# Kernel optimization log

Measured on AMD Instinct MI355X. Metric: run time of the kernel, lower is better.

## Reference

```python
import jax, jax.numpy as jnp
import numpy as np

B, H, W, C = 32, 32, 32, 512
N_GROUPS = 32
EPS = 1e-5


def group_norm(x, scale, bias, n_groups=N_GROUPS, eps=EPS):
    b, h, w, c = x.shape
    xg = x.reshape(b, h, w, n_groups, c // n_groups)
    mean = xg.mean(axis=(1, 2, 4), keepdims=True)
    var = xg.var(axis=(1, 2, 4), keepdims=True)
    xg = (xg - mean) * jax.lax.rsqrt(var + eps)
    return xg.reshape(b, h, w, c) * scale + bias


def setup_inputs() -> dict:
    key = jax.random.key(0)
    ks = jax.random.split(key, 8)
    x = jax.random.normal(ks[0], (B, H, W, C), dtype=jnp.float32)
    t = jax.random.normal(ks[1], (B,), dtype=jnp.float32)
    gn_scale = jnp.ones((C,), jnp.float32)
    gn_bias = jnp.zeros((C,), jnp.float32)
    w_qkv = jax.random.normal(ks[2], (C, 3 * C), dtype=jnp.float32) / np.sqrt(C)
    b_qkv = jnp.zeros((3 * C,), jnp.float32)
    w_out = jax.random.normal(ks[3], (C, C), dtype=jnp.float32) / np.sqrt(C)
    b_out = jnp.zeros((C,), jnp.float32)
    return {"x": x, "t": t, "gn_scale": gn_scale, "gn_bias": gn_bias,
            "w_qkv": w_qkv, "b_qkv": b_qkv, "w_out": w_out, "b_out": b_out}


def reference(x, t, gn_scale, gn_bias, w_qkv, b_qkv, w_out, b_out):
    b, h, w, c = x.shape
    z = group_norm(x, gn_scale, gn_bias)
    qkv = jnp.einsum('bhwc,cd->bhwd', z, w_qkv) + b_qkv  # [b,h,w,3C]
    q, k, v = jnp.split(qkv, 3, axis=-1)
    # single-head spatial attention over all h*w positions
    attn = jnp.einsum('bhwc,bHWc->bhwHW', q, k) / jnp.sqrt(jnp.asarray(c, x.dtype))
    attn = jax.nn.softmax(attn.reshape(b, h, w, h * w), axis=-1)
    attn = attn.reshape(b, h, w, h, w)
    scores = jnp.einsum('bhwHW,bHWc->bhwc', attn, v)
    scores = jnp.einsum('bhwc,cd->bhwd', scores, w_out) + b_out
    return x + scores
```

## Files before the change

### kernel.cpp

```cpp
#include <hip/hip_runtime.h>

typedef unsigned short u16;
typedef short bf16x8 __attribute__((ext_vector_type(8)));
typedef float f32x4 __attribute__((ext_vector_type(4)));

__device__ __forceinline__ u16 f2bf(float f) {
  union { float f; unsigned u; } c; c.f = f;
  unsigned r = (c.u + 0x7FFFu + ((c.u >> 16) & 1u)) >> 16;
  return (u16)r;
}
__device__ __forceinline__ float bf2f(u16 h) {
  union { unsigned u; float f; } c; c.u = ((unsigned)h) << 16;
  return c.f;
}
__device__ __forceinline__ void gload16(const void* g, void* l) {
  __builtin_amdgcn_global_load_lds(
      (const __attribute__((address_space(1))) unsigned*)g,
      (__attribute__((address_space(3))) unsigned*)l, 16, 0, 0);
}

__global__ __launch_bounds__(256) void prep_weights(
    const float* __restrict__ w_qkv, const float* __restrict__ w_out,
    u16* __restrict__ wqkvT, u16* __restrict__ woutT) {
  int i = blockIdx.x * 256 + threadIdx.x;
  const int T1 = 1536 * 512;
  if (i < T1) {
    int n = i >> 9, c = i & 511;
    wqkvT[i] = f2bf(w_qkv[(size_t)c * 1536 + n]);
  } else {
    int j = i - T1;
    int n = j >> 9, c = j & 511;
    woutT[j] = f2bf(w_out[(size_t)c * 512 + n]);
  }
}

__global__ __launch_bounds__(256) void groupnorm_k(
    const float* __restrict__ x, const float* __restrict__ scale,
    const float* __restrict__ bias, u16* __restrict__ z) {
  const int blk = blockIdx.x, b = blk >> 5, g = blk & 31;
  const float* xb = x + (size_t)b * 524288 + g * 16;
  u16* zb = z + (size_t)b * 524288 + g * 16;
  const int tid = threadIdx.x, lane = tid & 63, wid = tid >> 6;

  float4 vv[16];
  float s = 0.f, ss = 0.f;
#pragma unroll
  for (int i = 0; i < 16; ++i) {
    int e = (i * 256 + tid) * 4;
    int hw = e >> 4, j = e & 15;
    vv[i] = *(const float4*)&xb[(size_t)hw * 512 + j];
    s += vv[i].x + vv[i].y + vv[i].z + vv[i].w;
    ss += vv[i].x * vv[i].x + vv[i].y * vv[i].y + vv[i].z * vv[i].z + vv[i].w * vv[i].w;
  }
#pragma unroll
  for (int off = 32; off; off >>= 1) {
    s += __shfl_xor(s, off);
    ss += __shfl_xor(ss, off);
  }
  __shared__ float rs[4], rq[4];
  if (!lane) { rs[wid] = s; rq[wid] = ss; }
  __syncthreads();
  float S_ = rs[0] + rs[1] + rs[2] + rs[3];
  float Q_ = rq[0] + rq[1] + rq[2] + rq[3];
  const float inv_n = 1.f / 16384.f;
  float mean = S_ * inv_n;
  float var = Q_ * inv_n - mean * mean;
  float rstd = rsqrtf(var + 1e-5f);

  int j0 = (tid * 4) & 15;
  float sc0 = scale[g * 16 + j0 + 0] * rstd, sc1 = scale[g * 16 + j0 + 1] * rstd;
  float sc2 = scale[g * 16 + j0 + 2] * rstd, sc3 = scale[g * 16 + j0 + 3] * rstd;
  float bi0 = bias[g * 16 + j0 + 0] - mean * sc0, bi1 = bias[g * 16 + j0 + 1] - mean * sc1;
  float bi2 = bias[g * 16 + j0 + 2] - mean * sc2, bi3 = bias[g * 16 + j0 + 3] - mean * sc3;
#pragma unroll
  for (int i = 0; i < 16; ++i) {
    int e = (i * 256 + tid) * 4;
    int hw = e >> 4, j = e & 15;
    ushort4 o;
    o.x = f2bf(vv[i].x * sc0 + bi0);
    o.y = f2bf(vv[i].y * sc1 + bi1);
    o.z = f2bf(vv[i].z * sc2 + bi2);
    o.w = f2bf(vv[i].w * sc3 + bi3);
    *(ushort4*)&zb[(size_t)hw * 512 + j] = o;
  }
}

#define QSCALE 0.04419417382415922f

template <int EPI>
__global__ __launch_bounds__(512, 2) void gemm_ring(
    const u16* __restrict__ A, const u16* __restrict__ Bt,
    int gx, int gxy, int N, int K,
    int sched, int sp1, int sp2,
    long long sAb, long long sBb, long long sCb,
    const float* __restrict__ bias, const float* __restrict__ resid,
    u16* __restrict__ qb, u16* __restrict__ kb, u16* __restrict__ vt,
    u16* __restrict__ outb, float* __restrict__ outf) {
  const int orig = blockIdx.x;
  const int xcd = orig & 7, jj = orig >> 3;
  int id;
  if (sched == 0) {
    int pan = jj % gx, loc = jj / gx;
    id = (xcd * sp1 + loc) * gx + pan;
  } else {
    int tile = jj % gxy, bl = jj / gxy;
    id = (xcd * sp2 + bl) * gxy + tile;
  }
  const int z = id / gxy;
  const int r2 = id - z * gxy;
  const int by = r2 / gx, bx = r2 - by * gx;

  const u16* Ab = A + (size_t)z * sAb;
  const u16* Bb = Bt + (size_t)z * sBb;

  __shared__ u16 As[4][8192];
  __shared__ u16 Bs[4][8192];

  const int tid = threadIdx.x;
  const int lane = tid & 63, wid = tid >> 6;
  const int wm = wid & 1, wn = wid >> 1;
  const int l15 = lane & 15, l4 = lane >> 4;
  const int m0 = by * 256, n0 = bx * 256;

  const int lrs = tid >> 3;
  const int g0 = (tid & 7) ^ (lrs & 7);
  const int ra = (lrs << 1) | (g0 >> 2);
  const int ko = (g0 & 3) << 3;

  const int lrb = l15 >> 1;
  const int gg = ((l15 & 1) << 2) | l4;
  const int gsw = gg ^ lrb;
  const int aoff = wm * 4096 + lrb * 64 + gsw * 8;
  const int boff = (wn >> 1) * 4096 + (wn & 1) * 2048 + lrb * 64 + gsw * 8;

  f32x4 acc[8][4];
#pragma unroll
  for (int i = 0; i < 8; ++i)
#pragma unroll
    for (int j = 0; j < 4; ++j)
#pragma unroll
      for (int r = 0; r < 4; ++r) acc[i][j][r] = 0.f;

  const int NT = K >> 5;

  auto stA = [&](int sb, int t2) {
    const u16* s0 = Ab + (size_t)(m0 + ra) * K + t2 * 32 + ko;
    const u16* s1 = Ab + (size_t)(m0 + 128 + ra) * K + t2 * 32 + ko;
    gload16(s0, &As[sb][tid * 8]);
    gload16(s1, &As[sb][4096 + tid * 8]);
  };
  auto stB = [&](int sb, int t2) {
    const u16* s0 = Bb + (size_t)(n0 + ra) * K + t2 * 32 + ko;
    const u16* s1 = Bb + (size_t)(n0 + 128 + ra) * K + t2 * 32 + ko;
    gload16(s0, &Bs[sb][tid * 8]);
    gload16(s1, &Bs[sb][4096 + tid * 8]);
  };

#define TILE_BODY(P, TT, DOSTG, WN)                                            \
  do {                                                                         \
    if (DOSTG) { stA(((P) + 3) & 3, (TT) + 3); stB(((P) + 3) & 3, (TT) + 3); } \
    bf16x8 bq[4], af0[4], af1[4];                                              \
    _Pragma("unroll") for (int ni = 0; ni < 4; ++ni)                           \
        bq[ni] = *(const bf16x8*)&Bs[P][boff + ni * 512];                      \
    _Pragma("unroll") for (int i = 0; i < 4; ++i)                              \
        af0[i] = *(const bf16x8*)&As[P][aoff + i * 512];                       \
    _Pragma("unroll") for (int i = 0; i < 4; ++i)                              \
        af1[i] = *(const bf16x8*)&As[P][aoff + 2048 + i * 512];                \
    __builtin_amdgcn_s_setprio(1);                                             \
    _Pragma("unroll") for (int i = 0; i < 4; ++i)                              \
        _Pragma("unroll") for (int ni = 0; ni < 4; ++ni)                       \
            acc[i][ni] = __builtin_amdgcn_mfma_f32_16x16x32_bf16(              \
                af0[i], bq[ni], acc[i][ni], 0, 0, 0);                          \
    _Pragma("unroll") for (int i = 0; i < 4; ++i)                              \
        _Pragma("unroll") for (int ni = 0; ni < 4; ++ni)                       \
            acc[4 + i][ni] = __builtin_amdgcn_mfma_f32_16x16x32_bf16(          \
                af1[i], bq[ni], acc[4 + i][ni], 0, 0, 0);                      \
    __builtin_amdgcn_s_setprio(0);                                             \
    if ((WN) == 8) asm volatile("s_waitcnt vmcnt(8)" ::: "memory");            \
    else if ((WN) == 4) asm volatile("s_waitcnt vmcnt(4)" ::: "memory");       \
    else if ((WN) == 0) asm volatile("s_waitcnt vmcnt(0)" ::: "memory");       \
    if ((WN) >= -1) __builtin_amdgcn_s_barrier();                              \
  } while (0)

  stA(0, 0); stB(0, 0);
  stA(1, 1); stB(1, 1);
  stA(2, 2); stB(2, 2);
  asm volatile("s_waitcnt vmcnt(8)" ::: "memory");
  __builtin_amdgcn_s_barrier();

  int t = 0;
  for (; t + 7 < NT; t += 4) {
    TILE_BODY(0, t, 1, 8);
    TILE_BODY(1, t + 1, 1, 8);
    TILE_BODY(2, t + 2, 1, 8);
    TILE_BODY(3, t + 3, 1, 8);
  }
  TILE_BODY(0, t, 1, 8);
  TILE_BODY(1, t + 1, 0, 4);
  TILE_BODY(2, t + 2, 0, 0);
  TILE_BODY(3, t + 3, 0, -2);

#undef TILE_BODY

  if (EPI == 0) {
#pragma unroll
    for (int mi = 0; mi < 8; ++mi) {
#pragma unroll
      for (int ni = 0; ni < 4; ++ni) {
        const int gr0 = m0 + wm * 128 + mi * 16 + l4 * 4;
        const int gc = n0 + wn * 64 + ni * 16 + l15;
        const int bsel = gc >> 9, cin = gc & 511;
        const float bs = bias[gc];
        if (bsel < 2) {
          u16* dst = bsel ? kb : qb;
#pragma unroll
          for (int r = 0; r < 4; ++r) {
            float vvv = acc[mi][ni][r] + bs;
            if (bsel == 0) vvv *= QSCALE;
            dst[(size_t)(gr0 + r) * 512 + cin] = f2bf(vvv);
          }
        } else {
          ushort4 o;
          o.x = f2bf(acc[mi][ni][0] + bs);
          o.y = f2bf(acc[mi][ni][1] + bs);
          o.z = f2bf(acc[mi][ni][2] + bs);
          o.w = f2bf(acc[mi][ni][3] + bs);
          const int bb = gr0 >> 10, p = gr0 & 1023;
          *(ushort4*)&vt[(size_t)bb * 524288 + (size_t)cin * 1024 + p] = o;
        }
      }
    }
  } else {
#pragma unroll
    for (int mi = 0; mi < 8; ++mi) {
#pragma unroll
      for (int ni = 0; ni < 4; ++ni) {
        const int gr0 = m0 + wm * 128 + mi * 16 + l4 * 4;
        const int gc = n0 + wn * 64 + ni * 16 + l15;
#pragma unroll
        for (int r = 0; r < 4; ++r)
          outf[(size_t)(gr0 + r) * N + gc] =
              acc[mi][ni][r] + bias[gc] + resid[(size_t)(gr0 + r) * N + gc];
      }
    }
  }
}

__global__ __launch_bounds__(512, 2) void flash_k(
    const u16* __restrict__ qg, const u16* __restrict__ kg,
    const u16* __restrict__ vtg, u16* __restrict__ Og) {
  __shared__ u16 Ks[2][32 * 512];
  __shared__ u16 Ps[2][128 * 40];
  __shared__ float rsumS[128];

  const int tid = threadIdx.x, lane = tid & 63, wid = tid >> 6;
  const int l15 = lane & 15, l4 = lane >> 4;
  const int orig = blockIdx.x;
  const int xcd = orig & 7, jj = orig >> 3;
  const int z = xcd * 4 + (jj & 3);
  const int qb0 = jj >> 2;

  const u16* qz = qg + (size_t)(z * 1024 + qb0 * 128) * 512;
  const u16* kz = kg + (size_t)z * 1024 * 512;
  const u16* vz = vtg + (size_t)z * 512 * 1024;

  const int krow_ = tid >> 6;
  const int kgr = tid & 63;
  const int kgs = (kgr & 56) | ((kgr & 7) ^ (krow_ & 7));

  auto stageK = [&](int t, int buf) {
    const u16* src = kz + ((size_t)t * 32 + krow_) * 512 + kgs * 8;
#pragma unroll
    for (int s = 0; s < 4; ++s)
      gload16(src + (size_t)s * 8 * 512, &Ks[buf][s * 4096 + tid * 8]);
  };

  const int dbase = wid * 64;
  bf16x8 vcur[4], vnxt[4];
  auto loadV = [&](int t, bf16x8* dst) {
#pragma unroll
    for (int nf = 0; nf < 4; ++nf)
      dst[nf] = *(const bf16x8*)&vz[(size_t)(dbase + nf * 16 + l15) * 1024 + t * 32 + l4 * 8];
  };

  bf16x8 qf[16];
#pragma unroll
  for (int kf = 0; kf < 16; ++kf)
    qf[kf] = *(const bf16x8*)&qz[(size_t)(wid * 16 + l15) * 512 + kf * 32 + l4 * 8];

  f32x4 oacc[8][4];
#pragma unroll
  for (int i = 0; i < 8; ++i)
#pragma unroll
    for (int j = 0; j < 4; ++j)
#pragma unroll
      for (int r = 0; r < 4; ++r) oacc[i][j][r] = 0.f;
  float rsum[4] = {0.f, 0.f, 0.f, 0.f};

  stageK(0, 0);
  loadV(0, vcur);
  asm volatile("s_waitcnt vmcnt(4)" ::: "memory");
  __builtin_amdgcn_s_barrier();

  for (int t = 0; t < 32; ++t) {
    const int cur = t & 1;
    const bool pre = (t + 1 < 32);
    if (pre) { stageK(t + 1, cur ^ 1); loadV(t + 1, vnxt); }

    f32x4 sacc[2];
#pragma unroll
    for (int nf = 0; nf < 2; ++nf)
#pragma unroll
      for (int r = 0; r < 4; ++r) sacc[nf][r] = 0.f;
#pragma unroll
    for (int kf = 0; kf < 16; ++kf) {
#pragma unroll
      for (int nf = 0; nf < 2; ++nf) {
        const int kvr = nf * 16 + l15;
        const int g = kf * 4 + l4;
        const int gs = (g & 56) | ((g & 7) ^ (kvr & 7));
        const bf16x8 bfr = *(const bf16x8*)&Ks[cur][kvr * 512 + gs * 8];
        sacc[nf] = __builtin_amdgcn_mfma_f32_16x16x32_bf16(qf[kf], bfr, sacc[nf], 0, 0, 0);
      }
    }

#pragma unroll
    for (int nf = 0; nf < 2; ++nf)
#pragma unroll
      for (int r = 0; r < 4; ++r) {
        const float e = __expf(sacc[nf][r]);
        rsum[r] += e;
        Ps[cur][(wid * 16 + l4 * 4 + r) * 40 + nf * 16 + l15] = f2bf(e);
      }

    if (pre) asm volatile("s_waitcnt vmcnt(4)" ::: "memory");
    __builtin_amdgcn_s_barrier();

    __builtin_amdgcn_s_setprio(1);
#pragma unroll
    for (int mi = 0; mi < 8; ++mi) {
      const bf16x8 pa = *(const bf16x8*)&Ps[cur][(mi * 16 + l15) * 40 + l4 * 8];
#pragma unroll
      for (int nf = 0; nf < 4; ++nf)
        oacc[mi][nf] = __builtin_amdgcn_mfma_f32_16x16x32_bf16(pa, vcur[nf], oacc[mi][nf], 0, 0, 0);
    }
    __builtin_amdgcn_s_setprio(0);

    if (pre) {
#pragma unroll
      for (int nf = 0; nf < 4; ++nf) vcur[nf] = vnxt[nf];
    }
  }

#pragma unroll
  for (int r = 0; r < 4; ++r) {
    float v = rsum[r];
    v += __shfl_xor(v, 1);
    v += __shfl_xor(v, 2);
    v += __shfl_xor(v, 4);
    v += __shfl_xor(v, 8);
    if (l15 == 0) rsumS[wid * 16 + l4 * 4 + r] = 1.0f / v;
  }
  __syncthreads();

  u16* ob = Og + (size_t)(z * 1024 + qb0 * 128) * 512;
#pragma unroll
  for (int mi = 0; mi < 8; ++mi) {
#pragma unroll
    for (int r = 0; r < 4; ++r) {
      const int q = mi * 16 + l4 * 4 + r;
      const float inv = rsumS[q];
#pragma unroll
      for (int nf = 0; nf < 4; ++nf)
        ob[(size_t)q * 512 + dbase + nf * 16 + l15] = f2bf(oacc[mi][nf][r] * inv);
    }
  }
}

extern "C" void kernel_launch(void* const* d_in, const int* in_sizes, int n_in,
                              void* d_out, int out_size, void* d_ws, size_t ws_size,
                              hipStream_t stream) {
  const float* x = (const float*)d_in[0];
  const float* gn_scale = (const float*)d_in[2];
  const float* gn_bias = (const float*)d_in[3];
  const float* w_qkv = (const float*)d_in[4];
  const float* b_qkv = (const float*)d_in[5];
  const float* w_out = (const float*)d_in[6];
  const float* b_out = (const float*)d_in[7];
  float* out = (float*)d_out;

  char* ws = (char*)d_ws;
  const size_t MB = 1024ull * 1024ull;
  u16* qb = (u16*)(ws + 0 * MB);
  u16* kb = (u16*)(ws + 32 * MB);
  u16* vt = (u16*)(ws + 64 * MB);
  u16* zO = (u16*)(ws + 128 * MB);
  u16* wqkvT = (u16*)(ws + 224 * MB);
  u16* woutT = (u16*)(ws + 226 * MB);

  prep_weights<<<4096, 256, 0, stream>>>(w_qkv, w_out, wqkvT, woutT);
  groupnorm_k<<<1024, 256, 0, stream>>>(x, gn_scale, gn_bias, zO);

  gemm_ring<0><<<768, 512, 0, stream>>>(
      zO, wqkvT, 6, 768, 1536, 512, 0, 16, 0, 0, 0, 0, b_qkv, nullptr,
      qb, kb, vt, nullptr, nullptr);

  flash_k<<<256, 512, 0, stream>>>(qb, kb, vt, zO);

  gemm_ring<2><<<256, 512, 0, stream>>>(
      zO, woutT, 2, 256, 512, 512, 0, 16, 0, 0, 0, 0, b_out, x,
      nullptr, nullptr, nullptr, nullptr, out);
}
```

Baseline: 235.0 us.

## Software-pipeline attention loop so QK of tile t overlaps PV of tile t-1

Restructures the attention main loop so that each iteration computes the QK scores for the current K tile and the P·V product for the previous tile's probabilities. This lets the exp/softmax writes and the P·V MFMAs of neighbouring tiles interleave without waiting on each other. The V register double buffer now ping-pongs between two named arrays through a two-way unrolled macro body, which removes the per-iteration register copy. A peeled prologue and epilogue handle the first QK-only step and the final P·V. The extra unrolling may raise register pressure and lengthen the code.

```diff
diff --git a/kernel.cpp b/kernel.cpp
--- a/kernel.cpp
+++ b/kernel.cpp
@@ -276,8 +276,8 @@
   };
 
   const int dbase = wid * 64;
-  bf16x8 vcur[4], vnxt[4];
-  auto loadV = [&](int t, bf16x8* dst) {
+  bf16x8 va[4], vb[4];
+  auto loadV = [&](int t, bf16x8 (&dst)[4]) {
 #pragma unroll
     for (int nf = 0; nf < 4; ++nf)
       dst[nf] = *(const bf16x8*)&vz[(size_t)(dbase + nf * 16 + l15) * 1024 + t * 32 + l4 * 8];
@@ -298,59 +298,65 @@
   float rsum[4] = {0.f, 0.f, 0.f, 0.f};
 
   stageK(0, 0);
-  loadV(0, vcur);
+  loadV(0, vb);
   asm volatile("s_waitcnt vmcnt(4)" ::: "memory");
   __builtin_amdgcn_s_barrier();
 
-  for (int t = 0; t < 32; ++t) {
-    const int cur = t & 1;
-    const bool pre = (t + 1 < 32);
-    if (pre) { stageK(t + 1, cur ^ 1); loadV(t + 1, vnxt); }
-
-    f32x4 sacc[2];
-#pragma unroll
-    for (int nf = 0; nf < 2; ++nf)
-#pragma unroll
-      for (int r = 0; r < 4; ++r) sacc[nf][r] = 0.f;
-#pragma unroll
-    for (int kf = 0; kf < 16; ++kf) {
-#pragma unroll
-      for (int nf = 0; nf < 2; ++nf) {
-        const int kvr = nf * 16 + l15;
-        const int g = kf * 4 + l4;
-        const int gs = (g & 56) | ((g & 7) ^ (kvr & 7));
-        const bf16x8 bfr = *(const bf16x8*)&Ks[cur][kvr * 512 + gs * 8];
-        sacc[nf] = __builtin_amdgcn_mfma_f32_16x16x32_bf16(qf[kf], bfr, sacc[nf], 0, 0, 0);
-      }
-    }
-
-#pragma unroll
-    for (int nf = 0; nf < 2; ++nf)
-#pragma unroll
-      for (int r = 0; r < 4; ++r) {
-        const float e = __expf(sacc[nf][r]);
-        rsum[r] += e;
-        Ps[cur][(wid * 16 + l4 * 4 + r) * 40 + nf * 16 + l15] = f2bf(e);
-      }
-
-    if (pre) asm volatile("s_waitcnt vmcnt(4)" ::: "memory");
-    __builtin_amdgcn_s_barrier();
-
-    __builtin_amdgcn_s_setprio(1);
-#pragma unroll
-    for (int mi = 0; mi < 8; ++mi) {
-      const bf16x8 pa = *(const bf16x8*)&Ps[cur][(mi * 16 + l15) * 40 + l4 * 8];
-#pragma unroll
-      for (int nf = 0; nf < 4; ++nf)
-        oacc[mi][nf] = __builtin_amdgcn_mfma_f32_16x16x32_bf16(pa, vcur[nf], oacc[mi][nf], 0, 0, 0);
-    }
-    __builtin_amdgcn_s_setprio(0);
-
-    if (pre) {
-#pragma unroll
-      for (int nf = 0; nf < 4; ++nf) vcur[nf] = vnxt[nf];
-    }
-  }
+#define FBODY(I, VPV, DOPV, PRE)                                               \
+  do {                                                                         \
+    const int cur = (I) & 1;                                                   \
+    if (PRE) stageK((I) + 1, cur ^ 1);                                         \
+    f32x4 sacc[2];                                                             \
+    _Pragma("unroll") for (int nf = 0; nf < 2; ++nf)                           \
+      _Pragma("unroll") for (int r = 0; r < 4; ++r) sacc[nf][r] = 0.f;         \
+    __builtin_amdgcn_s_setprio(1);                                             \
+    _Pragma("unroll") for (int kf = 0; kf < 16; ++kf)                          \
+      _Pragma("unroll") for (int nf = 0; nf < 2; ++nf) {                       \
+        const int kvr = nf * 16 + l15;                                         \
+        const int g = kf * 4 + l4;                                             \
+        const int gs = (g & 56) | ((g & 7) ^ (kvr & 7));                       \
+        const bf16x8 bfr = *(const bf16x8*)&Ks[cur][kvr * 512 + gs * 8];       \
+        sacc[nf] = __builtin_amdgcn_mfma_f32_16x16x32_bf16(qf[kf], bfr,        \
+                                                           sacc[nf], 0, 0, 0);\
+      }                                                                        \
+    if (DOPV) {                                                                \
+      _Pragma("unroll") for (int mi = 0; mi < 8; ++mi) {                       \
+        const bf16x8 pa =                                                      \
+            *(const bf16x8*)&Ps[cur ^ 1][(mi * 16 + l15) * 40 + l4 * 8];       \
+        _Pragma("unroll") for (int nf = 0; nf < 4; ++nf)                       \
+          oacc[mi][nf] = __builtin_amdgcn_mfma_f32_16x16x32_bf16(              \
+              pa, VPV[nf], oacc[mi][nf], 0, 0, 0);                             \
+      }                                                                        \
+    }                                                                          \
+    __builtin_amdgcn_s_setprio(0);                                             \
+    if (PRE) loadV((I) + 1, VPV);                                              \
+    _Pragma("unroll") for (int nf = 0; nf < 2; ++nf)                           \
+      _Pragma("unroll") for (int r = 0; r < 4; ++r) {                          \
+        const float e = __expf(sacc[nf][r]);                                   \
+        rsum[r] += e;                                                          \
+        Ps[cur][(wid * 16 + l4 * 4 + r) * 40 + nf * 16 + l15] = f2bf(e);       \
+      }                                                                        \
+    if (PRE) asm volatile("s_waitcnt vmcnt(4)" ::: "memory");                  \
+    __builtin_amdgcn_s_barrier();                                              \
+  } while (0)
+
+  FBODY(0, va, 0, 1);
+  for (int t = 1; t < 31; t += 2) {
+    FBODY(t, vb, 1, 1);
+    FBODY(t + 1, va, 1, 1);
+  }
+  FBODY(31, vb, 1, 0);
+#undef FBODY
+
+  __builtin_amdgcn_s_setprio(1);
+#pragma unroll
+  for (int mi = 0; mi < 8; ++mi) {
+    const bf16x8 pa = *(const bf16x8*)&Ps[1][(mi * 16 + l15) * 40 + l4 * 8];
+#pragma unroll
+    for (int nf = 0; nf < 4; ++nf)
+      oacc[mi][nf] = __builtin_amdgcn_mfma_f32_16x16x32_bf16(pa, va[nf], oacc[mi][nf], 0, 0, 0);
+  }
+  __builtin_amdgcn_s_setprio(0);
 
 #pragma unroll
   for (int r = 0; r < 4; ++r) {
```

Result: slower. 316.2 us (+34.6%).
